# Performance work log

Measured on AMD Instinct MI355X. Metric: run time of the kernel, lower is better.

The kernel has to match this reference:

```python
import jax, jax.numpy as jnp
import numpy as np


def setup_inputs() -> dict:
    key = jax.random.key(0)
    N, D = 131072, 128
    x = jax.random.normal(key, (N, D), dtype=jnp.float32)
    return {"x": x, "k": 1024, "niters": 10}


def reference(x, k, niters):
    """Lloyd's k-means, Euclidean metric. Returns (clusters, centroids, n_points).

    Matches torch semantics: clusters are the assignments computed at the START
    of the last iteration (against the previous centroids); centroids/n_points
    reflect the update performed in that last iteration. Empty clusters divide
    by zero (-> inf/nan), same as the torch code.
    """
    K = int(k)
    x_sq = jnp.sum(x * x, axis=-1)  # [N], constant across iterations
    c0 = x[:K]

    def step(centroids, _):
        d = (x_sq[:, None]
             - 2.0 * jnp.einsum('nd,kd->nk', x, centroids)
             + jnp.sum(centroids * centroids, axis=-1)[None, :])
        clusters = jnp.argmin(d, axis=1)  # [N] int32
        sums = jax.ops.segment_sum(x, clusters, num_segments=K)  # [K, D] scatter-add
        counts = jax.ops.segment_sum(jnp.ones((x.shape[0],), x.dtype), clusters,
                                     num_segments=K)  # [K] bincount
        new_centroids = sums / counts[:, None]
        return new_centroids, (clusters, counts)

    centroids, (clusters_hist, counts_hist) = jax.lax.scan(step, c0, None, length=int(niters))
    return clusters_hist[-1].astype(jnp.int64), centroids, counts_hist[-1]
```

## Files before the change

kernel.cpp:

```cpp
#include <hip/hip_runtime.h>
#include <math.h>

#define DIM 128
#define KC 1024
#define NITER 10
#define BM 128
#define NB 512
#define THRESH 0.01f

typedef __bf16 bf16x8 __attribute__((ext_vector_type(8)));
typedef float f32x4 __attribute__((ext_vector_type(4)));

__device__ __forceinline__ unsigned short bf16rne(float f) {
    unsigned int u = __float_as_uint(f);
    unsigned int r = (u + 0x7FFFu + ((u >> 16) & 1u)) >> 16;
    return (unsigned short)r;
}

__device__ __forceinline__ bf16x8 pack_hi8(const float* fv, unsigned short* hs) {
    bf16x8 out;
    #pragma unroll
    for (int e = 0; e < 8; e++) {
        unsigned short h = bf16rne(fv[e]);
        hs[e] = h;
        out[e] = __builtin_bit_cast(__bf16, h);
    }
    return out;
}

__global__ void sq_np_kernel(const float* __restrict__ v, float* __restrict__ out, int rows) {
    int i = blockIdx.x * blockDim.x + threadIdx.x;
    if (i >= rows) return;
    const float4* row = (const float4*)(v + (size_t)i * DIM);
    float r[8];
    {
        float4 a = row[0], b = row[1];
        r[0] = __fmul_rn(a.x, a.x); r[1] = __fmul_rn(a.y, a.y);
        r[2] = __fmul_rn(a.z, a.z); r[3] = __fmul_rn(a.w, a.w);
        r[4] = __fmul_rn(b.x, b.x); r[5] = __fmul_rn(b.y, b.y);
        r[6] = __fmul_rn(b.z, b.z); r[7] = __fmul_rn(b.w, b.w);
    }
    #pragma unroll
    for (int blk = 1; blk < 16; blk++) {
        float4 a = row[blk * 2], b = row[blk * 2 + 1];
        r[0] = __fadd_rn(r[0], __fmul_rn(a.x, a.x));
        r[1] = __fadd_rn(r[1], __fmul_rn(a.y, a.y));
        r[2] = __fadd_rn(r[2], __fmul_rn(a.z, a.z));
        r[3] = __fadd_rn(r[3], __fmul_rn(a.w, a.w));
        r[4] = __fadd_rn(r[4], __fmul_rn(b.x, b.x));
        r[5] = __fadd_rn(r[5], __fmul_rn(b.y, b.y));
        r[6] = __fadd_rn(r[6], __fmul_rn(b.z, b.z));
        r[7] = __fadd_rn(r[7], __fmul_rn(b.w, b.w));
    }
    out[i] = __fadd_rn(__fadd_rn(__fadd_rn(r[0], r[1]), __fadd_rn(r[2], r[3])),
                       __fadd_rn(__fadd_rn(r[4], r[5]), __fadd_rn(r[6], r[7])));
}

__global__ __launch_bounds__(256, 3) void assign_mfma_kernel(
    const float* __restrict__ x,
    const ushort* __restrict__ centPh, const ushort* __restrict__ centPl,
    const float* __restrict__ csq,
    int* __restrict__ cl, int* __restrict__ fb_list, int* __restrict__ fbc)
{
    const int tid = threadIdx.x;
    const int lane = tid & 63;
    const int w = tid >> 6;
    const int bm = blockIdx.x * BM;
    const int row0 = bm + w * 32 + (lane & 15);
    const int ko = (lane >> 4) * 8;

    bf16x8 ah[2][4], al[2][4];
    #pragma unroll
    for (int m = 0; m < 2; m++) {
        const float* xr = x + (size_t)(row0 + m * 16) * DIM;
        #pragma unroll
        for (int dt = 0; dt < 4; dt++) {
            float4 a = *(const float4*)(xr + dt * 32 + ko);
            float4 b = *(const float4*)(xr + dt * 32 + ko + 4);
            float fv[8] = {a.x, a.y, a.z, a.w, b.x, b.y, b.z, b.w};
            unsigned short hs[8];
            ah[m][dt] = pack_hi8(fv, hs);
            bf16x8 lo;
            #pragma unroll
            for (int e = 0; e < 8; e++) {
                float rem = __fsub_rn(fv[e], __uint_as_float(((unsigned int)hs[e]) << 16));
                lo[e] = __builtin_bit_cast(__bf16, bf16rne(rem));
            }
            al[m][dt] = lo;
        }
    }

    float best1[8], best2[8];
    int bidx[8];
    int nanf = 0;
    #pragma unroll
    for (int s = 0; s < 8; s++) { best1[s] = INFINITY; best2[s] = INFINITY; bidx[s] = 0; }

    const ushort* pb = centPh + lane * 8;
    const ushort* qb = centPl + lane * 8;
    int kk = lane & 15;

    for (int kt = 0; kt < KC / 16; kt++) {
        const ushort* pk = pb + (size_t)kt * 2048;
        const ushort* qk = qb + (size_t)kt * 2048;
        bf16x8 bh0 = *(const bf16x8*)(pk);
        bf16x8 bh1 = *(const bf16x8*)(pk + 512);
        bf16x8 bh2 = *(const bf16x8*)(pk + 1024);
        bf16x8 bh3 = *(const bf16x8*)(pk + 1536);
        bf16x8 bl0 = *(const bf16x8*)(qk);
        bf16x8 bl1 = *(const bf16x8*)(qk + 512);
        bf16x8 bl2 = *(const bf16x8*)(qk + 1024);
        bf16x8 bl3 = *(const bf16x8*)(qk + 1536);

        f32x4 a0 = (f32x4){0.f, 0.f, 0.f, 0.f};
        f32x4 a1 = (f32x4){0.f, 0.f, 0.f, 0.f};
#define DT(BH, BL, D)                                                      \
        a0 = __builtin_amdgcn_mfma_f32_16x16x32_bf16(ah[0][D], BH, a0, 0, 0, 0); \
        a1 = __builtin_amdgcn_mfma_f32_16x16x32_bf16(ah[1][D], BH, a1, 0, 0, 0); \
        a0 = __builtin_amdgcn_mfma_f32_16x16x32_bf16(ah[0][D], BL, a0, 0, 0, 0); \
        a1 = __builtin_amdgcn_mfma_f32_16x16x32_bf16(ah[1][D], BL, a1, 0, 0, 0); \
        a0 = __builtin_amdgcn_mfma_f32_16x16x32_bf16(al[0][D], BH, a0, 0, 0, 0); \
        a1 = __builtin_amdgcn_mfma_f32_16x16x32_bf16(al[1][D], BH, a1, 0, 0, 0);
        DT(bh0, bl0, 0)
        DT(bh1, bl1, 1)
        DT(bh2, bl2, 2)
        DT(bh3, bl3, 3)
#undef DT

        float cq = csq[kk];
        nanf |= (cq != cq) ? 1 : 0;
        #pragma unroll
        for (int q = 0; q < 4; q++) {
            {
                float d = __fmaf_rn(-2.f, a0[q], cq);
                bool lt = (d < best1[q]);
                best2[q] = fminf(best2[q], lt ? best1[q] : d);
                if (lt) { best1[q] = d; bidx[q] = kk; }
            }
            {
                int s = 4 + q;
                float d = __fmaf_rn(-2.f, a1[q], cq);
                bool lt = (d < best1[s]);
                best2[s] = fminf(best2[s], lt ? best1[s] : d);
                if (lt) { best1[s] = d; bidx[s] = kk; }
            }
        }
        kk += 16;
    }

    #pragma unroll
    for (int mask = 1; mask < 16; mask <<= 1) {
        #pragma unroll
        for (int s = 0; s < 8; s++) {
            float ob1 = __shfl_xor(best1[s], mask, 64);
            float ob2 = __shfl_xor(best2[s], mask, 64);
            int   oi  = __shfl_xor(bidx[s],  mask, 64);
            float nb2 = fminf(fminf(best2[s], ob2), fmaxf(best1[s], ob1));
            bool take = (ob1 < best1[s]) || (ob1 == best1[s] && oi < bidx[s]);
            if (take) { best1[s] = ob1; bidx[s] = oi; }
            best2[s] = nb2;
        }
    }

    int wnan = __any(nanf);
    if ((lane & 15) == 0) {
        int hi = lane >> 4;
        #pragma unroll
        for (int s = 0; s < 8; s++) {
            int p = bm + w * 32 + (s >> 2) * 16 + hi * 4 + (s & 3);
            bool fb = (wnan != 0) || !(best2[s] - best1[s] > THRESH);
            if (fb) { int pos = atomicAdd(fbc, 1); fb_list[pos] = p; }
            else cl[p] = bidx[s];
        }
    }
}

__device__ __forceinline__ bool better(float od, int oi, float md, int mi) {
    bool n1 = (md != md), n2 = (od != od);
    if (n1 && n2) return oi < mi;
    if (n2) return true;
    if (n1) return false;
    return (od < md) || (od == md && oi < mi);
}

__global__ __launch_bounds__(256) void fixup_kernel(
    const float* __restrict__ x, const float* __restrict__ centTf,
    const float* __restrict__ xsq, const float* __restrict__ csq,
    const int* __restrict__ fb_list, const int* __restrict__ fbc,
    int* __restrict__ cl)
{
    __shared__ float xs[16][DIM];
    __shared__ float xqs[16];
    __shared__ int   ids[16];
    __shared__ float wv[16][4];
    __shared__ int   wi[16][4];
    const int t = threadIdx.x;
    const int lane = t & 63, wid = t >> 6;
    const int cnt = fbc[0];
    for (int w = blockIdx.x * 16; w < cnt; w += gridDim.x * 16) {
        int np = cnt - w; if (np > 16) np = 16;
        __syncthreads();
        if (t < np) { int i = fb_list[w + t]; ids[t] = i; xqs[t] = xsq[i]; }
        __syncthreads();
        for (int e = t; e < np * DIM; e += 256) {
            int p = e >> 7, d = e & 127;
            xs[p][d] = x[(size_t)ids[p] * DIM + d];
        }
        __syncthreads();
        float S[16][4];
        #pragma unroll
        for (int p = 0; p < 16; p++)
            #pragma unroll
            for (int c = 0; c < 4; c++) S[p][c] = 0.f;
        #pragma unroll 4
        for (int d = 0; d < DIM; d++) {
            const float* row = centTf + (size_t)d * KC;
            float c0 = row[t], c1 = row[t + 256], c2 = row[t + 512], c3 = row[t + 768];
            #pragma unroll
            for (int p = 0; p < 16; p++) {
                float xv = xs[p][d];
                S[p][0] = fmaf(xv, c0, S[p][0]);
                S[p][1] = fmaf(xv, c1, S[p][1]);
                S[p][2] = fmaf(xv, c2, S[p][2]);
                S[p][3] = fmaf(xv, c3, S[p][3]);
            }
        }
        float q0 = csq[t], q1 = csq[t + 256], q2 = csq[t + 512], q3 = csq[t + 768];
        #pragma unroll
        for (int p = 0; p < 16; p++) {
            float xq = xqs[p];
            float bb = INFINITY; int bi = 0x7fffffff;
            float dd; int c;
            c = t;       dd = __fadd_rn(__fsub_rn(xq, __fmul_rn(2.f, S[p][0])), q0); if (better(dd, c, bb, bi)) { bb = dd; bi = c; }
            c = t + 256; dd = __fadd_rn(__fsub_rn(xq, __fmul_rn(2.f, S[p][1])), q1); if (better(dd, c, bb, bi)) { bb = dd; bi = c; }
            c = t + 512; dd = __fadd_rn(__fsub_rn(xq, __fmul_rn(2.f, S[p][2])), q2); if (better(dd, c, bb, bi)) { bb = dd; bi = c; }
            c = t + 768; dd = __fadd_rn(__fsub_rn(xq, __fmul_rn(2.f, S[p][3])), q3); if (better(dd, c, bb, bi)) { bb = dd; bi = c; }
            #pragma unroll
            for (int mask = 1; mask < 64; mask <<= 1) {
                float od = __shfl_xor(bb, mask, 64);
                int   oi = __shfl_xor(bi, mask, 64);
                if (better(od, oi, bb, bi)) { bb = od; bi = oi; }
            }
            if (lane == 0) { wv[p][wid] = bb; wi[p][wid] = bi; }
        }
        __syncthreads();
        if (t < np) {
            float bb = wv[t][0]; int bi = wi[t][0];
            #pragma unroll
            for (int r = 1; r < 4; r++)
                if (better(wv[t][r], wi[t][r], bb, bi)) { bb = wv[t][r]; bi = wi[t][r]; }
            cl[ids[t]] = bi;
        }
    }
}


__global__ __launch_bounds__(256) void bhist_kernel(const int* __restrict__ cl,
                                                    int* __restrict__ bhist, int n) {
    __shared__ int h[KC];
    int t = threadIdx.x;
    #pragma unroll
    for (int q = 0; q < KC / 256; q++) h[t + q * 256] = 0;
    __syncthreads();
    int i = blockIdx.x * 256 + t;
    if (i < n) atomicAdd(&h[cl[i]], 1);
    __syncthreads();
    int* row = bhist + (size_t)blockIdx.x * KC;
    #pragma unroll
    for (int q = 0; q < KC / 256; q++) row[t + q * 256] = h[t + q * 256];
}

__global__ __launch_bounds__(256) void colsum_kernel(const int* __restrict__ bhist,
                                                     int* __restrict__ cnt) {
    int k = blockIdx.x * 256 + threadIdx.x;
    int s = 0;
    for (int b = 0; b < NB; b++) s += bhist[(size_t)b * KC + k];
    cnt[k] = s;
}

__global__ void scan_kernel(const int* __restrict__ cnt, int* __restrict__ off) {
    __shared__ int s[KC];
    int t = threadIdx.x;
    s[t] = cnt[t];
    __syncthreads();
    for (int o = 1; o < KC; o <<= 1) {
        int v = (t >= o) ? s[t - o] : 0;
        __syncthreads();
        s[t] += v;
        __syncthreads();
    }
    off[t] = s[t] - cnt[t];
}

__global__ __launch_bounds__(256) void blockpfx_kernel(int* __restrict__ bhist,
                                                       const int* __restrict__ off) {
    int k = blockIdx.x * 256 + threadIdx.x;
    int run = off[k];
    for (int b = 0; b < NB; b++) {
        size_t idx = (size_t)b * KC + k;
        int t = bhist[idx];
        bhist[idx] = run;
        run += t;
    }
}

__global__ __launch_bounds__(256) void stable_scatter_kernel(
    const int* __restrict__ cl, const int* __restrict__ bhist,
    int* __restrict__ list, int n)
{
    __shared__ int cls[256];
    int t = threadIdx.x;
    int i = blockIdx.x * 256 + t;
    int c = (i < n) ? cl[i] : -1;
    cls[t] = c;
    __syncthreads();
    if (i >= n) return;
    int rank = 0;
    for (int j = 0; j < 256; j++)
        rank += (j < t && cls[j] == c) ? 1 : 0;
    list[bhist[(size_t)blockIdx.x * KC + c] + rank] = i;
}

#define CHUNK 512
__global__ __launch_bounds__(128) void sum_kernel(
    const float* __restrict__ x, const int* __restrict__ list,
    const int* __restrict__ off, const int* __restrict__ cnt,
    float* __restrict__ cent, ushort* __restrict__ centPh,
    ushort* __restrict__ centPl, float* __restrict__ centTf,
    float* __restrict__ countsF)
{
    __shared__ int sidx[CHUNK];
    int k = blockIdx.x;
    int d = threadIdx.x;
    int o = off[k], m = cnt[k];
    float s = 0.f;
    for (int base = 0; base < m; base += CHUNK) {
        int c = m - base; if (c > CHUNK) c = CHUNK;
        __syncthreads();
        for (int t = d; t < c; t += 128) sidx[t] = list[o + base + t];
        __syncthreads();
        int j = 0;
        for (; j + 16 <= c; j += 16) {
            float v[16];
            #pragma unroll
            for (int u = 0; u < 16; u++)
                v[u] = x[(size_t)sidx[j + u] * DIM + d];
            #pragma unroll
            for (int u = 0; u < 16; u++)
                s = __fadd_rn(s, v[u]);
        }
        for (; j < c; j++)
            s = __fadd_rn(s, x[(size_t)sidx[j] * DIM + d]);
    }
    float mv = __fdiv_rn(s, (float)m);
    cent[(size_t)k * DIM + d] = mv;
    centTf[(size_t)d * KC + k] = mv;
    unsigned short h = bf16rne(mv);
    unsigned short lo = bf16rne(__fsub_rn(mv, __uint_as_float(((unsigned int)h) << 16)));
    int pidx = (((k >> 4) * 4 + (d >> 5)) * 64 + ((k & 15) + 16 * ((d >> 3) & 3))) * 8 + (d & 7);
    centPh[pidx] = h;
    centPl[pidx] = lo;
    if (d == 0) countsF[k] = (float)m;
}

__global__ void init_centP_kernel(const float* __restrict__ x,
                                  ushort* __restrict__ centPh, ushort* __restrict__ centPl,
                                  float* __restrict__ centTf) {
    int i = blockIdx.x * 256 + threadIdx.x;
    if (i < KC * DIM) {
        int k = i >> 7, d = i & 127;
        float v = x[i];
        centTf[(size_t)d * KC + k] = v;
        unsigned short h = bf16rne(v);
        unsigned short lo = bf16rne(__fsub_rn(v, __uint_as_float(((unsigned int)h) << 16)));
        int pidx = (((k >> 4) * 4 + (d >> 5)) * 64 + ((k & 15) + 16 * ((d >> 3) & 3))) * 8 + (d & 7);
        centPh[pidx] = h;
        centPl[pidx] = lo;
    }
}

__global__ void cl2f_kernel(const int* __restrict__ cl, float* __restrict__ out, int n) {
    int i = blockIdx.x * 256 + threadIdx.x;
    if (i < n) out[i] = (float)cl[i];
}

extern "C" void kernel_launch(void* const* d_in, const int* in_sizes, int n_in,
                              void* d_out, int out_size, void* d_ws, size_t ws_size,
                              hipStream_t stream) {
    const float* x = (const float*)d_in[0];
    const int n = in_sizes[0] / DIM;

    float* clf     = (float*)d_out;
    float* cent    = clf + n;
    float* countsF = cent + KC * DIM;

    float* xsq   = (float*)d_ws;
    float* csq   = xsq + n;
    int*   cl    = (int*)(csq + KC);
    int*   list  = cl + n;
    int*   cnt   = list + n;
    int*   off   = cnt + KC;
    int*   bhist = off + KC;
    ushort* centPh = (ushort*)(bhist + (size_t)NB * KC);
    ushort* centPl = centPh + KC * DIM;
    int*   fbc   = (int*)(centPl + KC * DIM);
    float* centTf = (float*)bhist;

    hipMemcpyAsync(cent, x, (size_t)KC * DIM * sizeof(float),
                   hipMemcpyDeviceToDevice, stream);
    init_centP_kernel<<<(KC * DIM + 255) / 256, 256, 0, stream>>>(x, centPh, centPl, centTf);
    sq_np_kernel<<<(n + 255) / 256, 256, 0, stream>>>(x, xsq, n);

    for (int it = 0; it < NITER; it++) {
        sq_np_kernel<<<(KC + 255) / 256, 256, 0, stream>>>(cent, csq, KC);
        hipMemsetAsync(fbc, 0, 2 * sizeof(int), stream);
        assign_mfma_kernel<<<n / BM, 256, 0, stream>>>(x, centPh, centPl, csq,
                                                       cl, list, fbc);
        fixup_kernel<<<1024, 256, 0, stream>>>(x, centTf, xsq, csq, list, fbc, cl);
        bhist_kernel<<<NB, 256, 0, stream>>>(cl, bhist, n);
        colsum_kernel<<<KC / 256, 256, 0, stream>>>(bhist, cnt);
        scan_kernel<<<1, KC, 0, stream>>>(cnt, off);
        blockpfx_kernel<<<KC / 256, 256, 0, stream>>>(bhist, off);
        stable_scatter_kernel<<<NB, 256, 0, stream>>>(cl, bhist, list, n);
        sum_kernel<<<KC, DIM, 0, stream>>>(x, list, off, cnt, cent, centPh, centPl, centTf, countsF);
    }

    cl2f_kernel<<<(n + 255) / 256, 256, 0, stream>>>(cl, clf, n);
}
```

Measured before the change: 2.294 ms.

## Software-pipeline centroid loads in assign loop and fuse csq/fbc reset into kernels

The assign kernel's K-loop is unrolled by two and double-buffers the high-part centroid fragments, prefetching the next tile's loads while the current MFMAs run. The MFMA order is regrouped so all hi*hi and lo*hi products come before hi*lo. The per-iteration centroid-norm kernel and the fbc memset are removed: sum_kernel now computes csq from shared memory, and bhist/init kernels reset fbc. This cuts per-iteration launches but raises register pressure, and the changed accumulation order could shift near-tie assignments.

```diff
diff --git a/kernel.cpp b/kernel.cpp
--- a/kernel.cpp
+++ b/kernel.cpp
@@ -28,10 +28,8 @@
     return out;
 }
 
-__global__ void sq_np_kernel(const float* __restrict__ v, float* __restrict__ out, int rows) {
-    int i = blockIdx.x * blockDim.x + threadIdx.x;
-    if (i >= rows) return;
-    const float4* row = (const float4*)(v + (size_t)i * DIM);
+__device__ __forceinline__ float sq_np_row(const float* __restrict__ v) {
+    const float4* row = (const float4*)v;
     float r[8];
     {
         float4 a = row[0], b = row[1];
@@ -52,8 +50,14 @@
         r[6] = __fadd_rn(r[6], __fmul_rn(b.z, b.z));
         r[7] = __fadd_rn(r[7], __fmul_rn(b.w, b.w));
     }
-    out[i] = __fadd_rn(__fadd_rn(__fadd_rn(r[0], r[1]), __fadd_rn(r[2], r[3])),
-                       __fadd_rn(__fadd_rn(r[4], r[5]), __fadd_rn(r[6], r[7])));
+    return __fadd_rn(__fadd_rn(__fadd_rn(r[0], r[1]), __fadd_rn(r[2], r[3])),
+                     __fadd_rn(__fadd_rn(r[4], r[5]), __fadd_rn(r[6], r[7])));
+}
+
+__global__ void sq_np_kernel(const float* __restrict__ v, float* __restrict__ out, int rows) {
+    int i = blockIdx.x * blockDim.x + threadIdx.x;
+    if (i >= rows) return;
+    out[i] = sq_np_row(v + (size_t)i * DIM);
 }
 
 __global__ __launch_bounds__(256, 3) void assign_mfma_kernel(
@@ -98,55 +102,68 @@
 
     const ushort* pb = centPh + lane * 8;
     const ushort* qb = centPl + lane * 8;
-    int kk = lane & 15;
-
-    for (int kt = 0; kt < KC / 16; kt++) {
-        const ushort* pk = pb + (size_t)kt * 2048;
-        const ushort* qk = qb + (size_t)kt * 2048;
-        bf16x8 bh0 = *(const bf16x8*)(pk);
-        bf16x8 bh1 = *(const bf16x8*)(pk + 512);
-        bf16x8 bh2 = *(const bf16x8*)(pk + 1024);
-        bf16x8 bh3 = *(const bf16x8*)(pk + 1536);
-        bf16x8 bl0 = *(const bf16x8*)(qk);
-        bf16x8 bl1 = *(const bf16x8*)(qk + 512);
-        bf16x8 bl2 = *(const bf16x8*)(qk + 1024);
-        bf16x8 bl3 = *(const bf16x8*)(qk + 1536);
-
-        f32x4 a0 = (f32x4){0.f, 0.f, 0.f, 0.f};
-        f32x4 a1 = (f32x4){0.f, 0.f, 0.f, 0.f};
-#define DT(BH, BL, D)                                                      \
-        a0 = __builtin_amdgcn_mfma_f32_16x16x32_bf16(ah[0][D], BH, a0, 0, 0, 0); \
-        a1 = __builtin_amdgcn_mfma_f32_16x16x32_bf16(ah[1][D], BH, a1, 0, 0, 0); \
-        a0 = __builtin_amdgcn_mfma_f32_16x16x32_bf16(ah[0][D], BL, a0, 0, 0, 0); \
-        a1 = __builtin_amdgcn_mfma_f32_16x16x32_bf16(ah[1][D], BL, a1, 0, 0, 0); \
-        a0 = __builtin_amdgcn_mfma_f32_16x16x32_bf16(al[0][D], BH, a0, 0, 0, 0); \
-        a1 = __builtin_amdgcn_mfma_f32_16x16x32_bf16(al[1][D], BH, a1, 0, 0, 0);
-        DT(bh0, bl0, 0)
-        DT(bh1, bl1, 1)
-        DT(bh2, bl2, 2)
-        DT(bh3, bl3, 3)
-#undef DT
-
-        float cq = csq[kk];
-        nanf |= (cq != cq) ? 1 : 0;
-        #pragma unroll
-        for (int q = 0; q < 4; q++) {
-            {
-                float d = __fmaf_rn(-2.f, a0[q], cq);
-                bool lt = (d < best1[q]);
-                best2[q] = fminf(best2[q], lt ? best1[q] : d);
-                if (lt) { best1[q] = d; bidx[q] = kk; }
-            }
-            {
-                int s = 4 + q;
-                float d = __fmaf_rn(-2.f, a1[q], cq);
-                bool lt = (d < best1[s]);
-                best2[s] = fminf(best2[s], lt ? best1[s] : d);
-                if (lt) { best1[s] = d; bidx[s] = kk; }
-            }
-        }
-        kk += 16;
-    }
+
+#define MFMA_(A, B, C) __builtin_amdgcn_mfma_f32_16x16x32_bf16(A, B, C, 0, 0, 0)
+
+    bf16x8 bhP0 = *(const bf16x8*)(pb);
+    bf16x8 bhP1 = *(const bf16x8*)(pb + 512);
+    bf16x8 bhP2 = *(const bf16x8*)(pb + 1024);
+    bf16x8 bhP3 = *(const bf16x8*)(pb + 1536);
+    bf16x8 bhQ0, bhQ1, bhQ2, bhQ3;
+
+#define PHASE(KT, B0, B1, B2, B3, N0, N1, N2, N3)                            \
+    {                                                                        \
+        const ushort* qk = qb + (size_t)(KT) * 2048;                         \
+        bf16x8 bl0 = *(const bf16x8*)(qk);                                   \
+        bf16x8 bl1 = *(const bf16x8*)(qk + 512);                             \
+        bf16x8 bl2 = *(const bf16x8*)(qk + 1024);                            \
+        bf16x8 bl3 = *(const bf16x8*)(qk + 1536);                            \
+        const ushort* pn = pb + (size_t)((KT) + 1) * 2048;                   \
+        N0 = *(const bf16x8*)(pn);                                           \
+        N1 = *(const bf16x8*)(pn + 512);                                     \
+        N2 = *(const bf16x8*)(pn + 1024);                                    \
+        N3 = *(const bf16x8*)(pn + 1536);                                    \
+        f32x4 a0 = (f32x4){0.f, 0.f, 0.f, 0.f};                              \
+        f32x4 a1 = (f32x4){0.f, 0.f, 0.f, 0.f};                              \
+        a0 = MFMA_(ah[0][0], B0, a0);  a1 = MFMA_(ah[1][0], B0, a1);         \
+        a0 = MFMA_(ah[0][1], B1, a0);  a1 = MFMA_(ah[1][1], B1, a1);         \
+        a0 = MFMA_(ah[0][2], B2, a0);  a1 = MFMA_(ah[1][2], B2, a1);         \
+        a0 = MFMA_(ah[0][3], B3, a0);  a1 = MFMA_(ah[1][3], B3, a1);         \
+        a0 = MFMA_(al[0][0], B0, a0);  a1 = MFMA_(al[1][0], B0, a1);         \
+        a0 = MFMA_(al[0][1], B1, a0);  a1 = MFMA_(al[1][1], B1, a1);         \
+        a0 = MFMA_(al[0][2], B2, a0);  a1 = MFMA_(al[1][2], B2, a1);         \
+        a0 = MFMA_(al[0][3], B3, a0);  a1 = MFMA_(al[1][3], B3, a1);         \
+        a0 = MFMA_(ah[0][0], bl0, a0); a1 = MFMA_(ah[1][0], bl0, a1);        \
+        a0 = MFMA_(ah[0][1], bl1, a0); a1 = MFMA_(ah[1][1], bl1, a1);        \
+        a0 = MFMA_(ah[0][2], bl2, a0); a1 = MFMA_(ah[1][2], bl2, a1);        \
+        a0 = MFMA_(ah[0][3], bl3, a0); a1 = MFMA_(ah[1][3], bl3, a1);        \
+        int kk = (KT) * 16 + (lane & 15);                                    \
+        float cq = csq[kk];                                                  \
+        nanf |= (cq != cq) ? 1 : 0;                                          \
+        _Pragma("unroll")                                                    \
+        for (int q = 0; q < 4; q++) {                                        \
+            {                                                                \
+                float d = __fmaf_rn(-2.f, a0[q], cq);                        \
+                bool lt = (d < best1[q]);                                    \
+                best2[q] = fminf(best2[q], lt ? best1[q] : d);               \
+                if (lt) { best1[q] = d; bidx[q] = kk; }                      \
+            }                                                                \
+            {                                                                \
+                int s = 4 + q;                                               \
+                float d = __fmaf_rn(-2.f, a1[q], cq);                        \
+                bool lt = (d < best1[s]);                                    \
+                best2[s] = fminf(best2[s], lt ? best1[s] : d);               \
+                if (lt) { best1[s] = d; bidx[s] = kk; }                      \
+            }                                                                \
+        }                                                                    \
+    }
+
+    for (int kt = 0; kt < KC / 16; kt += 2) {
+        PHASE(kt,     bhP0, bhP1, bhP2, bhP3, bhQ0, bhQ1, bhQ2, bhQ3)
+        PHASE(kt + 1, bhQ0, bhQ1, bhQ2, bhQ3, bhP0, bhP1, bhP2, bhP3)
+    }
+#undef PHASE
+#undef MFMA_
 
     #pragma unroll
     for (int mask = 1; mask < 16; mask <<= 1) {
@@ -256,9 +273,11 @@
 
 
 __global__ __launch_bounds__(256) void bhist_kernel(const int* __restrict__ cl,
-                                                    int* __restrict__ bhist, int n) {
+                                                    int* __restrict__ bhist, int n,
+                                                    int* __restrict__ fbc) {
     __shared__ int h[KC];
     int t = threadIdx.x;
+    if (blockIdx.x == 0 && t == 0) { fbc[0] = 0; fbc[1] = 0; }
     #pragma unroll
     for (int q = 0; q < KC / 256; q++) h[t + q * 256] = 0;
     __syncthreads();
@@ -327,9 +346,9 @@
     const int* __restrict__ off, const int* __restrict__ cnt,
     float* __restrict__ cent, ushort* __restrict__ centPh,
     ushort* __restrict__ centPl, float* __restrict__ centTf,
-    float* __restrict__ countsF)
+    float* __restrict__ csq, float* __restrict__ countsF)
 {
-    __shared__ int sidx[CHUNK];
+    __attribute__((aligned(16))) __shared__ int sidx[CHUNK];
     int k = blockIdx.x;
     int d = threadIdx.x;
     int o = off[k], m = cnt[k];
@@ -361,12 +380,17 @@
     centPh[pidx] = h;
     centPl[pidx] = lo;
     if (d == 0) countsF[k] = (float)m;
+    __syncthreads();
+    ((float*)sidx)[d] = mv;
+    __syncthreads();
+    if (d == 0) csq[k] = sq_np_row((const float*)sidx);
 }
 
 __global__ void init_centP_kernel(const float* __restrict__ x,
                                   ushort* __restrict__ centPh, ushort* __restrict__ centPl,
-                                  float* __restrict__ centTf) {
+                                  float* __restrict__ centTf, int* __restrict__ fbc) {
     int i = blockIdx.x * 256 + threadIdx.x;
+    if (i == 0) { fbc[0] = 0; fbc[1] = 0; }
     if (i < KC * DIM) {
         int k = i >> 7, d = i & 127;
         float v = x[i];
@@ -408,21 +432,23 @@
 
     hipMemcpyAsync(cent, x, (size_t)KC * DIM * sizeof(float),
                    hipMemcpyDeviceToDevice, stream);
-    init_centP_kernel<<<(KC * DIM + 255) / 256, 256, 0, stream>>>(x, centPh, centPl, centTf);
+    init_centP_kernel<<<(KC * DIM + 255) / 256, 256, 0, stream>>>(x, centPh, centPl,
+                                                                  centTf, fbc);
     sq_np_kernel<<<(n + 255) / 256, 256, 0, stream>>>(x, xsq, n);
+    hipMemcpyAsync(csq, xsq, (size_t)KC * sizeof(float),
+                   hipMemcpyDeviceToDevice, stream);
 
     for (int it = 0; it < NITER; it++) {
-        sq_np_kernel<<<(KC + 255) / 256, 256, 0, stream>>>(cent, csq, KC);
-        hipMemsetAsync(fbc, 0, 2 * sizeof(int), stream);
         assign_mfma_kernel<<<n / BM, 256, 0, stream>>>(x, centPh, centPl, csq,
                                                        cl, list, fbc);
         fixup_kernel<<<1024, 256, 0, stream>>>(x, centTf, xsq, csq, list, fbc, cl);
-        bhist_kernel<<<NB, 256, 0, stream>>>(cl, bhist, n);
+        bhist_kernel<<<NB, 256, 0, stream>>>(cl, bhist, n, fbc);
         colsum_kernel<<<KC / 256, 256, 0, stream>>>(bhist, cnt);
         scan_kernel<<<1, KC, 0, stream>>>(cnt, off);
         blockpfx_kernel<<<KC / 256, 256, 0, stream>>>(bhist, off);
         stable_scatter_kernel<<<NB, 256, 0, stream>>>(cl, bhist, list, n);
-        sum_kernel<<<KC, DIM, 0, stream>>>(x, list, off, cnt, cent, centPh, centPl, centTf, countsF);
+        sum_kernel<<<KC, DIM, 0, stream>>>(x, list, off, cnt, cent, centPh, centPl,
+                                           centTf, csq, countsF);
     }
 
     cl2f_kernel<<<(n + 255) / 256, 256, 0, stream>>>(cl, clf, n);
```

Result: slower. 2.510 ms (+9.4%).
